# Kernel tuning notes

Measured on AMD Instinct MI355X. Metric: run time of the kernel, lower is better.

Reference implementation:

```python
import jax, jax.numpy as jnp
import numpy as np

C = 1024
H = 16
K = 2  # num_states
B, N = 4, 4096


def setup_inputs() -> dict:
    key = jax.random.key(0)
    ks_ = jax.random.split(key, 12)
    s = 1.0 / np.sqrt(C)
    inp = {
        "x": jax.random.normal(ks_[0], (B, N, C), dtype=jnp.float32),
        "Wq": jax.random.normal(ks_[1], (C, C), dtype=jnp.float32) * s,
        "bq": jnp.zeros((C,), dtype=jnp.float32),
        "Wk": jax.random.normal(ks_[2], (K, C, C), dtype=jnp.float32) * s,
        "bk": jnp.zeros((K, C), dtype=jnp.float32),
        "Wv": jax.random.normal(ks_[3], (K, C, C), dtype=jnp.float32) * s,
        "bv": jnp.zeros((K, C), dtype=jnp.float32),
        "Wo": jax.random.normal(ks_[4], (C, C), dtype=jnp.float32) * s,
        "bo": jnp.zeros((C,), dtype=jnp.float32),
        "ln_g": jnp.ones((C,), dtype=jnp.float32),
        "ln_b": jnp.zeros((C,), dtype=jnp.float32),
    }
    return inp


def _heads(t):
    # [..., n, (h d)] -> [..., h, n, d]
    shp = t.shape
    d = shp[-1] // H
    t = t.reshape(shp[:-1] + (H, d))
    return jnp.swapaxes(t, -2, -3)


def reference(x, Wq, bq, Wk, bk, Wv, bv, Wo, bo, ln_g, ln_b):
    dtype = x.dtype
    # residual single-layer projections (ResidualMLP with num_layers=-1)
    q = x + jnp.einsum('bnc,cd->bnd', x, Wq) + bq
    ks = x[None] + jnp.einsum('bnc,kcd->kbnd', x, Wk) + bk[:, None, None, :]
    vs = x[None] + jnp.einsum('bnc,kcd->kbnd', x, Wv) + bv[:, None, None, :]
    q = _heads(q)        # [b,h,n,d]
    ks = _heads(ks)      # [k,b,h,n,d]
    vs = _heads(vs)      # [k,b,h,n,d]
    scale = 1.0 / jnp.sqrt(jnp.asarray(N, dtype=jnp.float32))
    ks = ks.astype(jnp.float32) * scale
    vs = vs.astype(jnp.float32) * scale
    # per-state KV outer-products: [k,b,h,d,e]
    states = jnp.einsum('kbhnd,kbhne->kbhde', ks, vs)
    state = jnp.prod(states, axis=0)  # [b,h,d,e]
    out = jnp.einsum('bhnd,bhde->bhne', q.astype(jnp.float32), state)
    out = out.astype(dtype)
    # [b,h,n,d] -> [b,n,(h d)]
    out = jnp.swapaxes(out, 1, 2).reshape(x.shape[0], x.shape[1], C)
    # LayerNorm
    mu = jnp.mean(out, axis=-1, keepdims=True)
    var = jnp.var(out, axis=-1, keepdims=True)
    out = (out - mu) / jnp.sqrt(var + 1e-5) * ln_g + ln_b
    out = jnp.einsum('bnc,cd->bnd', out, Wo) + bo
    return out
```

## Files before the change

### kernel.cpp

```cpp
#include <hip/hip_runtime.h>
#include <hip/hip_bf16.h>

typedef __attribute__((ext_vector_type(8))) short bf16x8;
typedef __attribute__((ext_vector_type(4))) float f32x4;
typedef __attribute__((ext_vector_type(4))) short s16x4;

__device__ __forceinline__ short f2bf(float f) {
  union { float f; unsigned u; } v; v.f = f;
  unsigned r = v.u + 0x7fffu + ((v.u >> 16) & 1u);
  return (short)(r >> 16);
}

__device__ __forceinline__ float bf2f(short s) {
  union { float f; unsigned u; } v; v.u = ((unsigned)(unsigned short)s) << 16;
  return v.f;
}

#define GLD_LDS(g, l) __builtin_amdgcn_global_load_lds( \
    (const __attribute__((address_space(1))) void*)(g), \
    (__attribute__((address_space(3))) void*)(l), 16, 0, 0)

__global__ __launch_bounds__(256)
void convt_k(const float* __restrict__ x, short* __restrict__ xb,
             short* __restrict__ xbT, float* __restrict__ s) {
  __shared__ short tile[64][72];
  __shared__ float red[4][64];
  const int b = blockIdx.z;
  const int n0 = blockIdx.y * 64;
  const int c0 = blockIdx.x * 64;
  const int t = threadIdx.x;
  const int nl = t >> 4;
  const int c4 = (t & 15) << 2;
  const float* xp = x + ((size_t)b * 4096 + n0) * 1024 + c0;
#pragma unroll
  for (int i = 0; i < 4; ++i) {
    const int n = nl + 16 * i;
    const float4 v = *(const float4*)(xp + (size_t)n * 1024 + c4);
    s16x4 o;
    o[0] = f2bf(v.x); o[1] = f2bf(v.y); o[2] = f2bf(v.z); o[3] = f2bf(v.w);
    *(s16x4*)(&xb[((size_t)b * 4096 + n0 + n) * 1024 + c0 + c4]) = o;
    *(s16x4*)(&tile[n][c4]) = o;
  }
  __syncthreads();
  const int cll = t >> 4;
  const int n4 = (t & 15) << 2;
#pragma unroll
  for (int i = 0; i < 4; ++i) {
    const int c = cll + 16 * i;
    s16x4 o;
    o[0] = tile[n4 + 0][c]; o[1] = tile[n4 + 1][c];
    o[2] = tile[n4 + 2][c]; o[3] = tile[n4 + 3][c];
    *(s16x4*)(&xbT[((size_t)b * 1024 + c0 + c) * 4096 + n0 + n4]) = o;
  }
  const int part = t >> 6, col = t & 63;
  float cs = 0.f;
#pragma unroll
  for (int i = 0; i < 16; ++i) cs += bf2f(tile[part * 16 + i][col]);
  red[part][col] = cs;
  __syncthreads();
  if (part == 0)
    atomicAdd(&s[b * 1024 + c0 + col],
              red[0][col] + red[1][col] + red[2][col] + red[3][col]);
}

__global__ void twc_k(const float* __restrict__ Wq, const float* __restrict__ Wk,
                      const float* __restrict__ Wv, const float* __restrict__ Wo,
                      const float* __restrict__ lng, short* __restrict__ dst,
                      short* __restrict__ wqn) {
  __shared__ float tile[32][33];
  const int z = blockIdx.z;
  const float* src = (z == 0) ? Wq
                   : (z == 1) ? Wk
                   : (z == 2) ? (Wk + 1048576)
                   : (z == 3) ? Wv
                   : (z == 4) ? (Wv + 1048576)
                   : Wo;
  short* d = dst + (size_t)z * 1048576;
  const int tx = threadIdx.x, ty = threadIdx.y;
  const int c0 = blockIdx.y * 32, d0 = blockIdx.x * 32;
#pragma unroll
  for (int i = 0; i < 4; ++i) {
    const int cc = c0 + ty + i * 8;
    const float v = src[(size_t)cc * 1024 + d0 + tx];
    tile[ty + i * 8][tx] = v;
    if (z == 0)
      wqn[(size_t)cc * 1024 + d0 + tx] = f2bf(v + (cc == d0 + tx ? 1.0f : 0.0f));
  }
  __syncthreads();
#pragma unroll
  for (int i = 0; i < 4; ++i) {
    const int cc = c0 + tx;
    const int dd = d0 + ty + i * 8;
    float v = tile[tx][ty + i * 8];
    if (z < 5) {
      if (cc == dd) v += 1.0f;
    } else {
      v *= lng[cc];
    }
    d[(size_t)dd * 1024 + cc] = f2bf(v);
  }
}

__global__ __launch_bounds__(256)
void gemv_k(const short* __restrict__ wt, const float* __restrict__ s,
            float* __restrict__ u, float* __restrict__ w) {
  const int z = blockIdx.z, b = blockIdx.y;
  const int lane = threadIdx.x & 63, wid = threadIdx.x >> 6;
  const short* W = wt + ((size_t)(z + 1) << 20);
  const float* sb = s + b * 1024;
  float* outp = (z < 2) ? (u + (z * 4 + b) * 1024) : (w + ((z - 2) * 4 + b) * 1024);
#pragma unroll 1
  for (int it = 0; it < 16; ++it) {
    const int d = blockIdx.x * 64 + wid * 16 + it;
    const short* row = W + (size_t)d * 1024 + lane * 16;
    float acc = 0.f;
#pragma unroll
    for (int j = 0; j < 16; ++j) acc += bf2f(row[j]) * sb[lane * 16 + j];
#pragma unroll
    for (int o = 32; o > 0; o >>= 1) acc += __shfl_down(acc, o);
    if (lane == 0) outp[d] = acc;
  }
}

__global__ __launch_bounds__(256)
void ut_k(const float* __restrict__ Wo, const float* __restrict__ lng,
          const float* __restrict__ lnb, const float* __restrict__ bo,
          float* __restrict__ u, float* __restrict__ t) {
  const int dl = threadIdx.x & 63;
  const int dd = blockIdx.x * 64 + dl;
  const int part = threadIdx.x >> 6;
  float su = 0.f, st = 0.f;
  for (int c = part * 256; c < part * 256 + 256; ++c) {
    const float w = Wo[(size_t)c * 1024 + dd];
    su += lng[c] * w;
    st += lnb[c] * w;
  }
  __shared__ float rs[4][64], rt[4][64];
  rs[part][dl] = su; rt[part][dl] = st;
  __syncthreads();
  if (part == 0) {
    su = rs[0][dl] + rs[1][dl] + rs[2][dl] + rs[3][dl];
    st = rt[0][dl] + rt[1][dl] + rt[2][dl] + rt[3][dl];
    u[dd] = su;
    t[dd] = st + bo[dd];
  }
}

__global__ __launch_bounds__(512, 2)
void gram_k(const short* __restrict__ xbT, float* __restrict__ Pg) {
  extern __shared__ short lds[];
  const int tid = threadIdx.x;
  const int lane = tid & 63;
  const int wv = tid >> 6;
  const int wm = wv >> 2;
  const int wn = wv & 3;
  const int swz = ((blockIdx.x & 7) << 5) + (blockIdx.x >> 3);
  const int b = swz >> 6;
  const int kz = (swz >> 4) & 3;
  const int tl = swz & 15;
  const int bm0 = (tl >> 2) << 8, bn0 = (tl & 3) << 8;
  const int koff = kz << 10;
  const short* Ap = xbT + ((size_t)b << 22);
  float* po = Pg + ((size_t)((kz << 2) + b) << 20);

  const int lrow = ((lane >> 3) << 1) | ((lane >> 2) & 1);
  const int kc = ((lane & 3) ^ ((lane >> 3) & 3)) << 3;
  const int cl = lane & 15;
  const int khi = lane >> 4;

  f32x4 acc[8][4];
#pragma unroll
  for (int i = 0; i < 8; ++i)
#pragma unroll
    for (int j = 0; j < 4; ++j) acc[i][j] = f32x4{0.f, 0.f, 0.f, 0.f};

  auto stage = [&](int buf, int t) {
    const int k0 = koff + (t << 5) + kc;
    short* ab = lds + (buf << 14);
    short* bb = ab + 8192;
#pragma unroll
    for (int c = 0; c < 2; ++c) {
      const int un = wv * 2 + c;
      GLD_LDS(Ap + (size_t)(bm0 + (un << 4) + lrow) * 4096 + k0, ab + (un << 9));
      GLD_LDS(Ap + (size_t)(bn0 + (un << 4) + lrow) * 4096 + k0, bb + (un << 9));
    }
  };

  auto compute = [&](int buf) {
    const short* ab = lds + (buf << 14);
    const short* bb = ab + 8192;
    bf16x8 af[8], bfr[4];
#pragma unroll
    for (int i = 0; i < 8; ++i) {
      const int R = (wm << 7) + (i << 4) + cl;
      af[i] = *(const bf16x8*)(ab + (R << 5) + ((khi ^ ((R >> 1) & 3)) << 3));
    }
#pragma unroll
    for (int j = 0; j < 4; ++j) {
      const int C = (wn << 6) + (j << 4) + cl;
      bfr[j] = *(const bf16x8*)(bb + (C << 5) + ((khi ^ ((C >> 1) & 3)) << 3));
    }
#pragma unroll
    for (int i = 0; i < 8; ++i)
#pragma unroll
      for (int j = 0; j < 4; ++j)
        acc[i][j] = __builtin_amdgcn_mfma_f32_16x16x32_bf16(af[i], bfr[j], acc[i][j], 0, 0, 0);
  };

  stage(0, 0);
  stage(1, 1);
  asm volatile("s_waitcnt vmcnt(4)" ::: "memory");
  __builtin_amdgcn_s_barrier();
#pragma unroll 1
  for (int t = 0; t < 30; ++t) {
    stage((t + 2) & 3, t + 2);
    compute(t & 3);
    asm volatile("s_waitcnt vmcnt(4)" ::: "memory");
    __builtin_amdgcn_s_barrier();
  }
  compute(2);
  asm volatile("s_waitcnt vmcnt(0)" ::: "memory");
  __builtin_amdgcn_s_barrier();
  compute(3);

#pragma unroll
  for (int i = 0; i < 8; ++i)
#pragma unroll
    for (int j = 0; j < 4; ++j) {
      const int col = bn0 + (wn << 6) + (j << 4) + cl;
      const int rowb = bm0 + (wm << 7) + (i << 4) + (khi << 2);
#pragma unroll
      for (int r = 0; r < 4; ++r)
        po[(size_t)(rowb + r) * 1024 + col] = acc[i][j][r];
    }
}

__global__ __launch_bounds__(512, 2)
void oat_k(const short* __restrict__ xb, const short* __restrict__ Beff,
           const float* __restrict__ rq, short* __restrict__ oat,
           float* __restrict__ musum, float* __restrict__ sqsum) {
  extern __shared__ short lds[];
  const int tid = threadIdx.x;
  const int lane = tid & 63;
  const int wv = tid >> 6;
  const int wm = wv >> 2;
  const int wn = wv & 3;
  const int swz = ((blockIdx.x & 7) << 5) + (blockIdx.x >> 3);
  const int b = swz >> 6;
  const int tl = swz & 63;
  const int bm0 = (tl >> 2) << 8;
  const int bn0 = (tl & 3) << 8;
  const short* Ap = xb + ((size_t)b << 22);
  const short* Bp = Beff + ((size_t)b << 20);

  const int lrow = ((lane >> 3) << 1) | ((lane >> 2) & 1);
  const int kc = ((lane & 3) ^ ((lane >> 3) & 3)) << 3;
  const int cl = lane & 15;
  const int khi = lane >> 4;

  f32x4 acc[8][4];
#pragma unroll
  for (int i = 0; i < 8; ++i)
#pragma unroll
    for (int j = 0; j < 4; ++j) acc[i][j] = f32x4{0.f, 0.f, 0.f, 0.f};

  auto stage = [&](int buf, int t) {
    const int k0 = (t << 5) + kc;
    short* ab = lds + (buf << 14);
    short* bb = ab + 8192;
#pragma unroll
    for (int c = 0; c < 2; ++c) {
      const int un = wv * 2 + c;
      GLD_LDS(Ap + (size_t)(bm0 + (un << 4) + lrow) * 1024 + k0, ab + (un << 9));
      GLD_LDS(Bp + (size_t)(bn0 + (un << 4) + lrow) * 1024 + k0, bb + (un << 9));
    }
  };

  auto compute = [&](int buf) {
    const short* ab = lds + (buf << 14);
    const short* bb = ab + 8192;
    bf16x8 af[8], bfr[4];
#pragma unroll
    for (int i = 0; i < 8; ++i) {
      const int R = (wm << 7) + (i << 4) + cl;
      af[i] = *(const bf16x8*)(ab + (R << 5) + ((khi ^ ((R >> 1) & 3)) << 3));
    }
#pragma unroll
    for (int j = 0; j < 4; ++j) {
      const int C = (wn << 6) + (j << 4) + cl;
      bfr[j] = *(const bf16x8*)(bb + (C << 5) + ((khi ^ ((C >> 1) & 3)) << 3));
    }
#pragma unroll
    for (int i = 0; i < 8; ++i)
#pragma unroll
      for (int j = 0; j < 4; ++j)
        acc[i][j] = __builtin_amdgcn_mfma_f32_16x16x32_bf16(af[i], bfr[j], acc[i][j], 0, 0, 0);
  };

  stage(0, 0);
  stage(1, 1);
  asm volatile("s_waitcnt vmcnt(4)" ::: "memory");
  __builtin_amdgcn_s_barrier();
#pragma unroll 1
  for (int t = 0; t < 30; ++t) {
    stage((t + 2) & 3, t + 2);
    compute(t & 3);
    asm volatile("s_waitcnt vmcnt(4)" ::: "memory");
    __builtin_amdgcn_s_barrier();
  }
  compute(2);
  asm volatile("s_waitcnt vmcnt(0)" ::: "memory");
  __builtin_amdgcn_s_barrier();
  compute(3);

#pragma unroll
  for (int i = 0; i < 8; ++i) {
    const int rowb = bm0 + (wm << 7) + (i << 4) + (khi << 2);
    s16x4 pk[4];
#pragma unroll
    for (int j = 0; j < 4; ++j) {
      const int col = bn0 + (wn << 6) + (j << 4) + cl;
      const float rqc = rq[b * 1024 + col];
#pragma unroll
      for (int r = 0; r < 4; ++r) pk[j][r] = f2bf(acc[i][j][r] + rqc);
#pragma unroll
      for (int r = 0; r < 4; ++r)
        oat[(size_t)(b * 4096 + rowb + r) * 1024 + col] = pk[j][r];
    }
#pragma unroll
    for (int r = 0; r < 4; ++r) {
      float sv = 0.f, sq = 0.f;
#pragma unroll
      for (int j = 0; j < 4; ++j) {
        const float fv = bf2f(pk[j][r]);
        sv += fv; sq += fv * fv;
      }
#pragma unroll
      for (int m = 1; m < 16; m <<= 1) {
        sv += __shfl_xor(sv, m);
        sq += __shfl_xor(sq, m);
      }
      if (cl == 0) {
        atomicAdd(&musum[b * 4096 + rowb + r], sv);
        atomicAdd(&sqsum[b * 4096 + rowb + r], sq);
      }
    }
  }
}

__global__ __launch_bounds__(256)
void greduce_k(const float* __restrict__ Pg, short* __restrict__ G) {
  const int b = blockIdx.x >> 10;
  const int local = ((blockIdx.x & 1023) << 10) + (threadIdx.x << 2);
  float4 a = {0.f, 0.f, 0.f, 0.f};
#pragma unroll
  for (int kz = 0; kz < 4; ++kz) {
    const float4 v = *(const float4*)(Pg + (((size_t)((kz << 2) + b)) << 20) + local);
    a.x += v.x; a.y += v.y; a.z += v.z; a.w += v.w;
  }
  const float sc = 1.0f / 4096.0f;
  s16x4 o;
  o[0] = f2bf(a.x * sc); o[1] = f2bf(a.y * sc);
  o[2] = f2bf(a.z * sc); o[3] = f2bf(a.w * sc);
  *(s16x4*)(G + ((size_t)b << 20) + local) = o;
}

__global__ __launch_bounds__(256, 2)
void gemm128_k(const short* __restrict__ A, const short* __restrict__ Bt,
               short* __restrict__ out) {
  extern __shared__ short lds[];
  const int bid = blockIdx.x;
  const int swz = ((bid & 7) << 4) + (bid >> 3);
  const int bm0 = (swz >> 3) << 7;
  const int bn0 = (swz & 7) << 7;
  const short* Bp = Bt + ((size_t)blockIdx.y << 20);
  short* op = out + ((size_t)blockIdx.y << 21);
  const int tid = threadIdx.x, lane = tid & 63, wid = tid >> 6;
  const int wm = (wid >> 1) << 6, wn = (wid & 1) << 6;
  const int lrow = ((lane >> 3) << 1) | ((lane >> 2) & 1);
  const int kc = ((lane & 3) ^ ((lane >> 3) & 3)) << 3;
  const int cl = lane & 15, khi = lane >> 4;

  f32x4 acc[4][4];
#pragma unroll
  for (int i = 0; i < 4; ++i)
#pragma unroll
    for (int j = 0; j < 4; ++j) acc[i][j] = f32x4{0.f, 0.f, 0.f, 0.f};

  auto stage = [&](int buf, int t) {
    const int k0 = (t << 5) + kc;
    short* ab = lds + (buf << 13);
    short* bb = ab + 4096;
#pragma unroll
    for (int c = 0; c < 2; ++c) {
      const int un = wid * 2 + c;
      GLD_LDS(A + (size_t)(bm0 + (un << 4) + lrow) * 1024 + k0, ab + (un << 9));
      GLD_LDS(Bp + (size_t)(bn0 + (un << 4) + lrow) * 1024 + k0, bb + (un << 9));
    }
  };

  auto compute = [&](int buf) {
    const short* ab = lds + (buf << 13);
    const short* bb = ab + 4096;
    bf16x8 af[4], bfr[4];
#pragma unroll
    for (int i = 0; i < 4; ++i) {
      const int R = wm + (i << 4) + cl;
      af[i] = *(const bf16x8*)(ab + (R << 5) + ((khi ^ ((R >> 1) & 3)) << 3));
    }
#pragma unroll
    for (int j = 0; j < 4; ++j) {
      const int C = wn + (j << 4) + cl;
      bfr[j] = *(const bf16x8*)(bb + (C << 5) + ((khi ^ ((C >> 1) & 3)) << 3));
    }
#pragma unroll
    for (int i = 0; i < 4; ++i)
#pragma unroll
      for (int j = 0; j < 4; ++j)
        acc[i][j] = __builtin_amdgcn_mfma_f32_16x16x32_bf16(af[i], bfr[j], acc[i][j], 0, 0, 0);
  };

  stage(0, 0);
  stage(1, 1);
  asm volatile("s_waitcnt vmcnt(4)" ::: "memory");
  __builtin_amdgcn_s_barrier();
#pragma unroll 1
  for (int t = 0; t < 30; ++t) {
    stage((t + 2) & 3, t + 2);
    compute(t & 3);
    asm volatile("s_waitcnt vmcnt(4)" ::: "memory");
    __builtin_amdgcn_s_barrier();
  }
  compute(2);
  asm volatile("s_waitcnt vmcnt(0)" ::: "memory");
  __builtin_amdgcn_s_barrier();
  compute(3);

#pragma unroll
  for (int i = 0; i < 4; ++i)
#pragma unroll
    for (int j = 0; j < 4; ++j) {
      const int col = bn0 + wn + (j << 4) + cl;
      const int rowb = bm0 + wm + (i << 4) + (khi << 2);
#pragma unroll
      for (int r = 0; r < 4; ++r)
        op[(size_t)(rowb + r) * 1024 + col] = f2bf(acc[i][j][r]);
    }
}

__global__ __launch_bounds__(256)
void sw_k(const short* __restrict__ wt, const short* __restrict__ Tt,
          const float* __restrict__ u, const float* __restrict__ w,
          const float* __restrict__ bk, const float* __restrict__ bv,
          const short* __restrict__ wqn, const float* __restrict__ bq,
          short* __restrict__ Beff, float* __restrict__ rq) {
  __shared__ short Al[64 * 40];
  __shared__ short Bl[64 * 40];
  __shared__ short S[64][72];
  const int h = blockIdx.x & 15, b = blockIdx.x >> 4;
  const int tid = threadIdx.x, lane = tid & 63, wid = tid >> 6;
  const int srow = tid >> 2, sch = (tid & 3) << 3;
  const int cl = lane & 15, khi = lane >> 4;

  f32x4 acc2[2][4];
#pragma unroll
  for (int k = 0; k < 2; ++k)
#pragma unroll
    for (int j = 0; j < 4; ++j) acc2[k][j] = f32x4{0.f, 0.f, 0.f, 0.f};

#pragma unroll
  for (int k = 0; k < 2; ++k) {
    const short* Ap = wt + ((size_t)(1 + k) << 20) + ((size_t)(h * 64) << 10);
    const short* Bp = Tt + ((size_t)b << 21) + ((size_t)(k * 1024 + h * 64) << 10);
#pragma unroll 1
    for (int ns = 0; ns < 1024; ns += 32) {
      bf16x8 va = *(const bf16x8*)(Ap + ((size_t)srow << 10) + ns + sch);
      bf16x8 vb = *(const bf16x8*)(Bp + ((size_t)srow << 10) + ns + sch);
      __syncthreads();
      *(bf16x8*)(Al + srow * 40 + sch) = va;
      *(bf16x8*)(Bl + srow * 40 + sch) = vb;
      __syncthreads();
      bf16x8 a = *(const bf16x8*)(Al + (wid * 16 + cl) * 40 + (khi << 3));
#pragma unroll
      for (int j = 0; j < 4; ++j) {
        bf16x8 bb = *(const bf16x8*)(Bl + (j * 16 + cl) * 40 + (khi << 3));
        acc2[k][j] = __builtin_amdgcn_mfma_f32_16x16x32_bf16(a, bb, acc2[k][j], 0, 0, 0);
      }
    }
  }

  const int d0 = wid * 16 + (khi << 2);
  const float invN = 1.0f / 4096.0f;
#pragma unroll
  for (int j = 0; j < 4; ++j) {
    const int e = j * 16 + cl;
    s16x4 pk;
#pragma unroll
    for (int r = 0; r < 4; ++r) {
      const int d = d0 + r;
      float m[2];
#pragma unroll
      for (int k = 0; k < 2; ++k) {
        const float bkd = bk[k * 1024 + h * 64 + d];
        const float bve = bv[k * 1024 + h * 64 + e];
        const float ud = u[(k * 4 + b) * 1024 + h * 64 + d];
        const float we = w[(k * 4 + b) * 1024 + h * 64 + e];
        m[k] = acc2[k][j][r] + (ud * bve + bkd * we + 4096.f * bkd * bve) * invN;
      }
      pk[r] = f2bf(m[0] * m[1]);
    }
    *(s16x4*)(&S[e][d0]) = pk;
  }
  __syncthreads();

  if (wid == 0) {
    float acc = 0.f;
#pragma unroll 1
    for (int d = 0; d < 64; ++d) acc += bq[h * 64 + d] * bf2f(S[lane][d]);
    rq[b * 1024 + h * 64 + lane] = acc;
  }
  bf16x8 af[4][2];
#pragma unroll
  for (int mi = 0; mi < 4; ++mi)
#pragma unroll
    for (int kk = 0; kk < 2; ++kk)
      af[mi][kk] = *(const bf16x8*)(&S[mi * 16 + cl][kk * 32 + khi * 8]);
  const short* wq = wqn + h * 64;
  short* bdst = Beff + ((size_t)b << 20) + ((size_t)(h * 64) << 10);
#pragma unroll 1
  for (int nf = 0; nf < 16; ++nf) {
    const int c0 = wid * 256 + nf * 16;
    const bf16x8 bf0 = *(const bf16x8*)(wq + (size_t)(c0 + cl) * 1024 + khi * 8);
    const bf16x8 bf1 = *(const bf16x8*)(wq + (size_t)(c0 + cl) * 1024 + 32 + khi * 8);
    f32x4 a4[4];
#pragma unroll
    for (int mi = 0; mi < 4; ++mi) {
      a4[mi] = f32x4{0.f, 0.f, 0.f, 0.f};
      a4[mi] = __builtin_amdgcn_mfma_f32_16x16x32_bf16(af[mi][0], bf0, a4[mi], 0, 0, 0);
      a4[mi] = __builtin_amdgcn_mfma_f32_16x16x32_bf16(af[mi][1], bf1, a4[mi], 0, 0, 0);
    }
#pragma unroll
    for (int mi = 0; mi < 4; ++mi)
#pragma unroll
      for (int r = 0; r < 4; ++r)
        bdst[(size_t)(mi * 16 + khi * 4 + r) * 1024 + c0 + cl] = f2bf(a4[mi][r]);
  }
}

__global__ __launch_bounds__(512, 2)
void gemmo_k(const short* __restrict__ A, const short* __restrict__ WT,
             const float* __restrict__ musum, const float* __restrict__ sqsum,
             const float* __restrict__ uu, const float* __restrict__ tt,
             float* __restrict__ fout) {
  extern __shared__ short lds[];
  const int tid = threadIdx.x;
  const int lane = tid & 63;
  const int wv = tid >> 6;
  const int wm = wv >> 2;
  const int wn = wv & 3;
  const int swz = ((blockIdx.x & 7) << 5) + (blockIdx.x >> 3);
  const int bm0 = (swz >> 2) << 8;
  const int bn0 = (swz & 3) << 8;

  const int lrow = ((lane >> 3) << 1) | ((lane >> 2) & 1);
  const int kc = ((lane & 3) ^ ((lane >> 3) & 3)) << 3;
  const int cl = lane & 15;
  const int khi = lane >> 4;

  f32x4 acc[8][4];
#pragma unroll
  for (int i = 0; i < 8; ++i)
#pragma unroll
    for (int j = 0; j < 4; ++j) acc[i][j] = f32x4{0.f, 0.f, 0.f, 0.f};

  auto stage = [&](int buf, int t) {
    const int k0 = (t << 5) + kc;
    short* ab = lds + (buf << 14);
    short* bb = ab + 8192;
#pragma unroll
    for (int c = 0; c < 2; ++c) {
      const int un = wv * 2 + c;
      GLD_LDS(A + (size_t)(bm0 + (un << 4) + lrow) * 1024 + k0, ab + (un << 9));
      GLD_LDS(WT + (size_t)(bn0 + (un << 4) + lrow) * 1024 + k0, bb + (un << 9));
    }
  };

  auto compute = [&](int buf) {
    const short* ab = lds + (buf << 14);
    const short* bb = ab + 8192;
    bf16x8 af[8], bfr[4];
#pragma unroll
    for (int i = 0; i < 8; ++i) {
      const int R = (wm << 7) + (i << 4) + cl;
      af[i] = *(const bf16x8*)(ab + (R << 5) + ((khi ^ ((R >> 1) & 3)) << 3));
    }
#pragma unroll
    for (int j = 0; j < 4; ++j) {
      const int C = (wn << 6) + (j << 4) + cl;
      bfr[j] = *(const bf16x8*)(bb + (C << 5) + ((khi ^ ((C >> 1) & 3)) << 3));
    }
#pragma unroll
    for (int i = 0; i < 8; ++i)
#pragma unroll
      for (int j = 0; j < 4; ++j)
        acc[i][j] = __builtin_amdgcn_mfma_f32_16x16x32_bf16(af[i], bfr[j], acc[i][j], 0, 0, 0);
  };

  stage(0, 0);
  stage(1, 1);
  asm volatile("s_waitcnt vmcnt(4)" ::: "memory");
  __builtin_amdgcn_s_barrier();
#pragma unroll 1
  for (int t = 0; t < 30; ++t) {
    stage((t + 2) & 3, t + 2);
    compute(t & 3);
    asm volatile("s_waitcnt vmcnt(4)" ::: "memory");
    __builtin_amdgcn_s_barrier();
  }
  compute(2);
  asm volatile("s_waitcnt vmcnt(0)" ::: "memory");
  __builtin_amdgcn_s_barrier();
  compute(3);

#pragma unroll
  for (int i = 0; i < 8; ++i) {
    const int rowb = bm0 + (wm << 7) + (i << 4) + (khi << 2);
    const float4 ms = *(const float4*)(musum + rowb);
    const float4 qs = *(const float4*)(sqsum + rowb);
    float mu[4], rs[4];
    mu[0] = ms.x * (1.0f / 1024.0f); mu[1] = ms.y * (1.0f / 1024.0f);
    mu[2] = ms.z * (1.0f / 1024.0f); mu[3] = ms.w * (1.0f / 1024.0f);
    rs[0] = rsqrtf(fmaxf(qs.x * (1.0f / 1024.0f) - mu[0] * mu[0], 0.f) + 1e-5f);
    rs[1] = rsqrtf(fmaxf(qs.y * (1.0f / 1024.0f) - mu[1] * mu[1], 0.f) + 1e-5f);
    rs[2] = rsqrtf(fmaxf(qs.z * (1.0f / 1024.0f) - mu[2] * mu[2], 0.f) + 1e-5f);
    rs[3] = rsqrtf(fmaxf(qs.w * (1.0f / 1024.0f) - mu[3] * mu[3], 0.f) + 1e-5f);
#pragma unroll
    for (int j = 0; j < 4; ++j) {
      const int col = bn0 + (wn << 6) + (j << 4) + cl;
      const float uc = uu[col];
      const float tc = tt[col];
#pragma unroll
      for (int r = 0; r < 4; ++r)
        fout[(size_t)(rowb + r) * 1024 + col] = rs[r] * (acc[i][j][r] - mu[r] * uc) + tc;
    }
  }
}

extern "C" void kernel_launch(void* const* d_in, const int* in_sizes, int n_in,
                              void* d_out, int out_size, void* d_ws, size_t ws_size,
                              hipStream_t stream) {
  const float* x = (const float*)d_in[0];
  const float* Wq = (const float*)d_in[1];
  const float* bq = (const float*)d_in[2];
  const float* Wk = (const float*)d_in[3];
  const float* bk = (const float*)d_in[4];
  const float* Wv = (const float*)d_in[5];
  const float* bv = (const float*)d_in[6];
  const float* Wo = (const float*)d_in[7];
  const float* bo = (const float*)d_in[8];
  const float* lng = (const float*)d_in[9];
  const float* lnb = (const float*)d_in[10];

  char* ws = (char*)d_ws;
  short* xb = (short*)(ws + 0);
  short* wt = (short*)(ws + 33554432);
  short* wqn = (short*)(ws + 46137344);
  short* Beff = (short*)(ws + 48234496);
  float* rq = (float*)(ws + 56623104);
  float* musum = (float*)(ws + 56639488);
  float* sqsum = (float*)(ws + 56705024);
  float* s = (float*)(ws + 56770560);
  float* u = (float*)(ws + 56786944);
  float* w = (float*)(ws + 56819712);
  float* uu = (float*)(ws + 56852480);
  float* tt = (float*)(ws + 56856576);
  short* xbT = (short*)(ws + 79691776);
  short* Gt = (short*)(ws + 113246208);
  short* Tt = (short*)(ws + 121634816);
  float* Pg = (float*)(ws + 143351808);
  short* oat = xbT;

  hipMemsetAsync(musum, 0, 147456, stream);
  convt_k<<<dim3(16, 64, 4), 256, 0, stream>>>(x, xb, xbT, s);
  twc_k<<<dim3(32, 32, 6), dim3(32, 8), 0, stream>>>(Wq, Wk, Wv, Wo, lng, wt, wqn);
  gemv_k<<<dim3(16, 4, 4), 256, 0, stream>>>(wt, s, u, w);
  ut_k<<<16, 256, 0, stream>>>(Wo, lng, lnb, bo, uu, tt);

  gram_k<<<256, 512, 131072, stream>>>(xbT, Pg);
  greduce_k<<<4096, 256, 0, stream>>>(Pg, Gt);
  gemm128_k<<<dim3(128, 4), 256, 65536, stream>>>(wt + 3145728, Gt, Tt);
  sw_k<<<64, 256, 0, stream>>>(wt, Tt, u, w, bk, bv, wqn, bq, Beff, rq);

  oat_k<<<256, 512, 131072, stream>>>(xb, Beff, rq, oat, musum, sqsum);
  gemmo_k<<<256, 512, 131072, stream>>>(oat, wt + 5242880, musum, sqsum, uu, tt,
                                        (float*)d_out);
}
```

Measured before the change: 271.6 us.

## Unify GEMMs into 128x128 triple-buffered template; exploit Gram symmetry

Four 256x256-tile GEMM kernels using 512 threads and a 4-stage LDS ring are replaced by one templated 128x128-tile kernel. It uses 256 threads, a 3-stage ring, 48KB of LDS and a target of 3 blocks per CU, with a MODE parameter selecting the prologue and epilogue. The Gram kernel now computes only the upper-triangular tiles of the symmetric x^T x. The reduction kernel then sums the split-K partials per 64x64 tile and writes each off-diagonal tile's transpose through LDS. This raises block count and occupancy and roughly halves Gram MFMA work, at the cost of lower per-block reuse and more global traffic per FLOP.

Measured after the change: 278.3 us. +2.5%, slower.

```diff
diff --git a/kernel.cpp b/kernel.cpp
--- a/kernel.cpp
+++ b/kernel.cpp
@@ -146,62 +146,93 @@
   }
 }
 
-__global__ __launch_bounds__(512, 2)
-void gram_k(const short* __restrict__ xbT, float* __restrict__ Pg) {
+template <int MODE>
+__global__ __launch_bounds__(256, 3)
+void g128_k(const short* __restrict__ A0, const short* __restrict__ B0,
+            const float* __restrict__ cr0, const float* __restrict__ cr1,
+            float* __restrict__ musum, float* __restrict__ sqsum,
+            short* __restrict__ obf, float* __restrict__ of32) {
   extern __shared__ short lds[];
-  const int tid = threadIdx.x;
-  const int lane = tid & 63;
-  const int wv = tid >> 6;
-  const int wm = wv >> 2;
-  const int wn = wv & 3;
-  const int swz = ((blockIdx.x & 7) << 5) + (blockIdx.x >> 3);
-  const int b = swz >> 6;
-  const int kz = (swz >> 4) & 3;
-  const int tl = swz & 15;
-  const int bm0 = (tl >> 2) << 8, bn0 = (tl & 3) << 8;
-  const int koff = kz << 10;
-  const short* Ap = xbT + ((size_t)b << 22);
-  float* po = Pg + ((size_t)((kz << 2) + b) << 20);
-
+  const int tid = threadIdx.x, lane = tid & 63, wid = tid >> 6;
+  const int wm = (wid >> 1) << 6, wn = (wid & 1) << 6;
   const int lrow = ((lane >> 3) << 1) | ((lane >> 2) & 1);
   const int kc = ((lane & 3) ^ ((lane >> 3) & 3)) << 3;
-  const int cl = lane & 15;
-  const int khi = lane >> 4;
-
-  f32x4 acc[8][4];
-#pragma unroll
-  for (int i = 0; i < 8; ++i)
+  const int cl = lane & 15, khi = lane >> 4;
+
+  int bm0, bn0, koff = 0, b = 0, ld;
+  const short *Ap, *Bp;
+  if constexpr (MODE == 0) {
+    const int swz = (blockIdx.x & 7) * 72 + (blockIdx.x >> 3);
+    const int panel = swz / 36;
+    int uu2 = swz % 36;
+    b = panel >> 2;
+    const int kz = panel & 3;
+    int ti = 0;
+    while (uu2 >= 8 - ti) { uu2 -= 8 - ti; ++ti; }
+    const int tj = ti + uu2;
+    bm0 = ti << 7; bn0 = tj << 7;
+    koff = kz << 10; ld = 4096;
+    Ap = A0 + ((size_t)b << 22);
+    Bp = Ap;
+    of32 += ((size_t)((kz << 2) + b) << 20);
+  } else if constexpr (MODE == 1) {
+    const int swz = (blockIdx.x & 7) * 64 + (blockIdx.x >> 3);
+    b = swz >> 7;
+    const int tl = swz & 127;
+    bm0 = (tl >> 3) << 7; bn0 = (tl & 7) << 7;
+    ld = 1024;
+    Ap = A0;
+    Bp = B0 + ((size_t)b << 20);
+    obf += ((size_t)b << 21);
+  } else if constexpr (MODE == 2) {
+    const int swz = (blockIdx.x & 7) * 128 + (blockIdx.x >> 3);
+    b = swz >> 8;
+    const int tl = swz & 255;
+    bm0 = (tl >> 3) << 7; bn0 = (tl & 7) << 7;
+    ld = 1024;
+    Ap = A0 + ((size_t)b << 22);
+    Bp = B0 + ((size_t)b << 20);
+  } else {
+    const int swz = (blockIdx.x & 7) * 128 + (blockIdx.x >> 3);
+    bm0 = (swz >> 3) << 7; bn0 = (swz & 7) << 7;
+    ld = 1024;
+    Ap = A0; Bp = B0;
+  }
+
+  f32x4 acc[4][4];
+#pragma unroll
+  for (int i = 0; i < 4; ++i)
 #pragma unroll
     for (int j = 0; j < 4; ++j) acc[i][j] = f32x4{0.f, 0.f, 0.f, 0.f};
 
   auto stage = [&](int buf, int t) {
     const int k0 = koff + (t << 5) + kc;
-    short* ab = lds + (buf << 14);
-    short* bb = ab + 8192;
+    short* ab = lds + buf * 8192;
+    short* bb = ab + 4096;
 #pragma unroll
     for (int c = 0; c < 2; ++c) {
-      const int un = wv * 2 + c;
-      GLD_LDS(Ap + (size_t)(bm0 + (un << 4) + lrow) * 4096 + k0, ab + (un << 9));
-      GLD_LDS(Ap + (size_t)(bn0 + (un << 4) + lrow) * 4096 + k0, bb + (un << 9));
+      const int un = wid * 2 + c;
+      GLD_LDS(Ap + (size_t)(bm0 + (un << 4) + lrow) * ld + k0, ab + (un << 9));
+      GLD_LDS(Bp + (size_t)(bn0 + (un << 4) + lrow) * ld + k0, bb + (un << 9));
     }
   };
 
   auto compute = [&](int buf) {
-    const short* ab = lds + (buf << 14);
-    const short* bb = ab + 8192;
-    bf16x8 af[8], bfr[4];
-#pragma unroll
-    for (int i = 0; i < 8; ++i) {
-      const int R = (wm << 7) + (i << 4) + cl;
+    const short* ab = lds + buf * 8192;
+    const short* bb = ab + 4096;
+    bf16x8 af[4], bfr[4];
+#pragma unroll
+    for (int i = 0; i < 4; ++i) {
+      const int R = wm + (i << 4) + cl;
       af[i] = *(const bf16x8*)(ab + (R << 5) + ((khi ^ ((R >> 1) & 3)) << 3));
     }
 #pragma unroll
     for (int j = 0; j < 4; ++j) {
-      const int C = (wn << 6) + (j << 4) + cl;
+      const int C = wn + (j << 4) + cl;
       bfr[j] = *(const bf16x8*)(bb + (C << 5) + ((khi ^ ((C >> 1) & 3)) << 3));
     }
 #pragma unroll
-    for (int i = 0; i < 8; ++i)
+    for (int i = 0; i < 4; ++i)
 #pragma unroll
       for (int j = 0; j < 4; ++j)
         acc[i][j] = __builtin_amdgcn_mfma_f32_16x16x32_bf16(af[i], bfr[j], acc[i][j], 0, 0, 0);
@@ -213,239 +244,145 @@
   __builtin_amdgcn_s_barrier();
 #pragma unroll 1
   for (int t = 0; t < 30; ++t) {
-    stage((t + 2) & 3, t + 2);
-    compute(t & 3);
+    stage((t + 2) % 3, t + 2);
+    compute(t % 3);
     asm volatile("s_waitcnt vmcnt(4)" ::: "memory");
     __builtin_amdgcn_s_barrier();
   }
-  compute(2);
+  compute(0);
   asm volatile("s_waitcnt vmcnt(0)" ::: "memory");
   __builtin_amdgcn_s_barrier();
-  compute(3);
-
-#pragma unroll
-  for (int i = 0; i < 8; ++i)
-#pragma unroll
-    for (int j = 0; j < 4; ++j) {
-      const int col = bn0 + (wn << 6) + (j << 4) + cl;
-      const int rowb = bm0 + (wm << 7) + (i << 4) + (khi << 2);
-#pragma unroll
-      for (int r = 0; r < 4; ++r)
-        po[(size_t)(rowb + r) * 1024 + col] = acc[i][j][r];
-    }
-}
-
-__global__ __launch_bounds__(512, 2)
-void oat_k(const short* __restrict__ xb, const short* __restrict__ Beff,
-           const float* __restrict__ rq, short* __restrict__ oat,
-           float* __restrict__ musum, float* __restrict__ sqsum) {
-  extern __shared__ short lds[];
-  const int tid = threadIdx.x;
-  const int lane = tid & 63;
-  const int wv = tid >> 6;
-  const int wm = wv >> 2;
-  const int wn = wv & 3;
-  const int swz = ((blockIdx.x & 7) << 5) + (blockIdx.x >> 3);
-  const int b = swz >> 6;
-  const int tl = swz & 63;
-  const int bm0 = (tl >> 2) << 8;
-  const int bn0 = (tl & 3) << 8;
-  const short* Ap = xb + ((size_t)b << 22);
-  const short* Bp = Beff + ((size_t)b << 20);
-
-  const int lrow = ((lane >> 3) << 1) | ((lane >> 2) & 1);
-  const int kc = ((lane & 3) ^ ((lane >> 3) & 3)) << 3;
-  const int cl = lane & 15;
-  const int khi = lane >> 4;
-
-  f32x4 acc[8][4];
-#pragma unroll
-  for (int i = 0; i < 8; ++i)
-#pragma unroll
-    for (int j = 0; j < 4; ++j) acc[i][j] = f32x4{0.f, 0.f, 0.f, 0.f};
-
-  auto stage = [&](int buf, int t) {
-    const int k0 = (t << 5) + kc;
-    short* ab = lds + (buf << 14);
-    short* bb = ab + 8192;
-#pragma unroll
-    for (int c = 0; c < 2; ++c) {
-      const int un = wv * 2 + c;
-      GLD_LDS(Ap + (size_t)(bm0 + (un << 4) + lrow) * 1024 + k0, ab + (un << 9));
-      GLD_LDS(Bp + (size_t)(bn0 + (un << 4) + lrow) * 1024 + k0, bb + (un << 9));
-    }
-  };
-
-  auto compute = [&](int buf) {
-    const short* ab = lds + (buf << 14);
-    const short* bb = ab + 8192;
-    bf16x8 af[8], bfr[4];
-#pragma unroll
-    for (int i = 0; i < 8; ++i) {
-      const int R = (wm << 7) + (i << 4) + cl;
-      af[i] = *(const bf16x8*)(ab + (R << 5) + ((khi ^ ((R >> 1) & 3)) << 3));
-    }
-#pragma unroll
-    for (int j = 0; j < 4; ++j) {
-      const int C = (wn << 6) + (j << 4) + cl;
-      bfr[j] = *(const bf16x8*)(bb + (C << 5) + ((khi ^ ((C >> 1) & 3)) << 3));
-    }
-#pragma unroll
-    for (int i = 0; i < 8; ++i)
-#pragma unroll
-      for (int j = 0; j < 4; ++j)
-        acc[i][j] = __builtin_amdgcn_mfma_f32_16x16x32_bf16(af[i], bfr[j], acc[i][j], 0, 0, 0);
-  };
-
-  stage(0, 0);
-  stage(1, 1);
-  asm volatile("s_waitcnt vmcnt(4)" ::: "memory");
-  __builtin_amdgcn_s_barrier();
-#pragma unroll 1
-  for (int t = 0; t < 30; ++t) {
-    stage((t + 2) & 3, t + 2);
-    compute(t & 3);
-    asm volatile("s_waitcnt vmcnt(4)" ::: "memory");
-    __builtin_amdgcn_s_barrier();
-  }
-  compute(2);
-  asm volatile("s_waitcnt vmcnt(0)" ::: "memory");
-  __builtin_amdgcn_s_barrier();
-  compute(3);
-
-#pragma unroll
-  for (int i = 0; i < 8; ++i) {
-    const int rowb = bm0 + (wm << 7) + (i << 4) + (khi << 2);
-    s16x4 pk[4];
-#pragma unroll
-    for (int j = 0; j < 4; ++j) {
-      const int col = bn0 + (wn << 6) + (j << 4) + cl;
-      const float rqc = rq[b * 1024 + col];
-#pragma unroll
-      for (int r = 0; r < 4; ++r) pk[j][r] = f2bf(acc[i][j][r] + rqc);
-#pragma unroll
-      for (int r = 0; r < 4; ++r)
-        oat[(size_t)(b * 4096 + rowb + r) * 1024 + col] = pk[j][r];
-    }
-#pragma unroll
-    for (int r = 0; r < 4; ++r) {
-      float sv = 0.f, sq = 0.f;
+  compute(1);
+
+  if constexpr (MODE == 0) {
+#pragma unroll
+    for (int i = 0; i < 4; ++i)
 #pragma unroll
       for (int j = 0; j < 4; ++j) {
-        const float fv = bf2f(pk[j][r]);
-        sv += fv; sq += fv * fv;
-      }
-#pragma unroll
-      for (int m = 1; m < 16; m <<= 1) {
-        sv += __shfl_xor(sv, m);
-        sq += __shfl_xor(sq, m);
-      }
-      if (cl == 0) {
-        atomicAdd(&musum[b * 4096 + rowb + r], sv);
-        atomicAdd(&sqsum[b * 4096 + rowb + r], sq);
+        const int col = bn0 + wn + (j << 4) + cl;
+        const int rowb = bm0 + wm + (i << 4) + (khi << 2);
+#pragma unroll
+        for (int r = 0; r < 4; ++r)
+          of32[(size_t)(rowb + r) * 1024 + col] = acc[i][j][r];
+      }
+  } else if constexpr (MODE == 1) {
+#pragma unroll
+    for (int i = 0; i < 4; ++i)
+#pragma unroll
+      for (int j = 0; j < 4; ++j) {
+        const int col = bn0 + wn + (j << 4) + cl;
+        const int rowb = bm0 + wm + (i << 4) + (khi << 2);
+#pragma unroll
+        for (int r = 0; r < 4; ++r)
+          obf[(size_t)(rowb + r) * 1024 + col] = f2bf(acc[i][j][r]);
+      }
+  } else if constexpr (MODE == 2) {
+#pragma unroll
+    for (int i = 0; i < 4; ++i) {
+      const int rowb = bm0 + wm + (i << 4) + (khi << 2);
+      s16x4 pk[4];
+#pragma unroll
+      for (int j = 0; j < 4; ++j) {
+        const int col = bn0 + wn + (j << 4) + cl;
+        const float rqc = cr0[b * 1024 + col];
+#pragma unroll
+        for (int r = 0; r < 4; ++r) pk[j][r] = f2bf(acc[i][j][r] + rqc);
+#pragma unroll
+        for (int r = 0; r < 4; ++r)
+          obf[(size_t)(b * 4096 + rowb + r) * 1024 + col] = pk[j][r];
+      }
+#pragma unroll
+      for (int r = 0; r < 4; ++r) {
+        float sv = 0.f, sq = 0.f;
+#pragma unroll
+        for (int j = 0; j < 4; ++j) {
+          const float fv = bf2f(pk[j][r]);
+          sv += fv; sq += fv * fv;
+        }
+#pragma unroll
+        for (int m = 1; m < 16; m <<= 1) {
+          sv += __shfl_xor(sv, m);
+          sq += __shfl_xor(sq, m);
+        }
+        if (cl == 0) {
+          atomicAdd(&musum[b * 4096 + rowb + r], sv);
+          atomicAdd(&sqsum[b * 4096 + rowb + r], sq);
+        }
+      }
+    }
+  } else {
+#pragma unroll
+    for (int i = 0; i < 4; ++i) {
+      const int rowb = bm0 + wm + (i << 4) + (khi << 2);
+      const float4 ms = *(const float4*)(musum + rowb);
+      const float4 qs = *(const float4*)(sqsum + rowb);
+      float mu[4], rs[4];
+      mu[0] = ms.x * (1.0f / 1024.0f); mu[1] = ms.y * (1.0f / 1024.0f);
+      mu[2] = ms.z * (1.0f / 1024.0f); mu[3] = ms.w * (1.0f / 1024.0f);
+      rs[0] = rsqrtf(fmaxf(qs.x * (1.0f / 1024.0f) - mu[0] * mu[0], 0.f) + 1e-5f);
+      rs[1] = rsqrtf(fmaxf(qs.y * (1.0f / 1024.0f) - mu[1] * mu[1], 0.f) + 1e-5f);
+      rs[2] = rsqrtf(fmaxf(qs.z * (1.0f / 1024.0f) - mu[2] * mu[2], 0.f) + 1e-5f);
+      rs[3] = rsqrtf(fmaxf(qs.w * (1.0f / 1024.0f) - mu[3] * mu[3], 0.f) + 1e-5f);
+#pragma unroll
+      for (int j = 0; j < 4; ++j) {
+        const int col = bn0 + wn + (j << 4) + cl;
+        const float uc = cr0[col];
+        const float tc = cr1[col];
+#pragma unroll
+        for (int r = 0; r < 4; ++r)
+          of32[(size_t)(rowb + r) * 1024 + col] = rs[r] * (acc[i][j][r] - mu[r] * uc) + tc;
       }
     }
   }
 }
 
 __global__ __launch_bounds__(256)
-void greduce_k(const float* __restrict__ Pg, short* __restrict__ G) {
-  const int b = blockIdx.x >> 10;
-  const int local = ((blockIdx.x & 1023) << 10) + (threadIdx.x << 2);
-  float4 a = {0.f, 0.f, 0.f, 0.f};
+void gred_k(const float* __restrict__ Pg, short* __restrict__ G) {
+  __shared__ short tile[64][72];
+  const int bid = blockIdx.x;
+  const int b = bid / 136;
+  int u = bid % 136;
+  int ti = 0;
+  while (u >= 16 - ti) { u -= 16 - ti; ++ti; }
+  const int tj = ti + u;
+  const int r = threadIdx.x >> 2;
+  const int c0 = (threadIdx.x & 3) << 4;
+  float acc[16];
+#pragma unroll
+  for (int q = 0; q < 16; ++q) acc[q] = 0.f;
 #pragma unroll
   for (int kz = 0; kz < 4; ++kz) {
-    const float4 v = *(const float4*)(Pg + (((size_t)((kz << 2) + b)) << 20) + local);
-    a.x += v.x; a.y += v.y; a.z += v.z; a.w += v.w;
+    const float* p = Pg + (((size_t)((kz << 2) + b)) << 20)
+                   + (size_t)(ti * 64 + r) * 1024 + tj * 64 + c0;
+#pragma unroll
+    for (int q4 = 0; q4 < 4; ++q4) {
+      const float4 v = ((const float4*)p)[q4];
+      acc[q4 * 4 + 0] += v.x; acc[q4 * 4 + 1] += v.y;
+      acc[q4 * 4 + 2] += v.z; acc[q4 * 4 + 3] += v.w;
+    }
   }
   const float sc = 1.0f / 4096.0f;
-  s16x4 o;
-  o[0] = f2bf(a.x * sc); o[1] = f2bf(a.y * sc);
-  o[2] = f2bf(a.z * sc); o[3] = f2bf(a.w * sc);
-  *(s16x4*)(G + ((size_t)b << 20) + local) = o;
-}
-
-__global__ __launch_bounds__(256, 2)
-void gemm128_k(const short* __restrict__ A, const short* __restrict__ Bt,
-               short* __restrict__ out) {
-  extern __shared__ short lds[];
-  const int bid = blockIdx.x;
-  const int swz = ((bid & 7) << 4) + (bid >> 3);
-  const int bm0 = (swz >> 3) << 7;
-  const int bn0 = (swz & 7) << 7;
-  const short* Bp = Bt + ((size_t)blockIdx.y << 20);
-  short* op = out + ((size_t)blockIdx.y << 21);
-  const int tid = threadIdx.x, lane = tid & 63, wid = tid >> 6;
-  const int wm = (wid >> 1) << 6, wn = (wid & 1) << 6;
-  const int lrow = ((lane >> 3) << 1) | ((lane >> 2) & 1);
-  const int kc = ((lane & 3) ^ ((lane >> 3) & 3)) << 3;
-  const int cl = lane & 15, khi = lane >> 4;
-
-  f32x4 acc[4][4];
-#pragma unroll
-  for (int i = 0; i < 4; ++i)
-#pragma unroll
-    for (int j = 0; j < 4; ++j) acc[i][j] = f32x4{0.f, 0.f, 0.f, 0.f};
-
-  auto stage = [&](int buf, int t) {
-    const int k0 = (t << 5) + kc;
-    short* ab = lds + (buf << 13);
-    short* bb = ab + 4096;
-#pragma unroll
-    for (int c = 0; c < 2; ++c) {
-      const int un = wid * 2 + c;
-      GLD_LDS(A + (size_t)(bm0 + (un << 4) + lrow) * 1024 + k0, ab + (un << 9));
-      GLD_LDS(Bp + (size_t)(bn0 + (un << 4) + lrow) * 1024 + k0, bb + (un << 9));
-    }
-  };
-
-  auto compute = [&](int buf) {
-    const short* ab = lds + (buf << 13);
-    const short* bb = ab + 4096;
-    bf16x8 af[4], bfr[4];
-#pragma unroll
-    for (int i = 0; i < 4; ++i) {
-      const int R = wm + (i << 4) + cl;
-      af[i] = *(const bf16x8*)(ab + (R << 5) + ((khi ^ ((R >> 1) & 3)) << 3));
-    }
-#pragma unroll
-    for (int j = 0; j < 4; ++j) {
-      const int C = wn + (j << 4) + cl;
-      bfr[j] = *(const bf16x8*)(bb + (C << 5) + ((khi ^ ((C >> 1) & 3)) << 3));
-    }
-#pragma unroll
-    for (int i = 0; i < 4; ++i)
-#pragma unroll
-      for (int j = 0; j < 4; ++j)
-        acc[i][j] = __builtin_amdgcn_mfma_f32_16x16x32_bf16(af[i], bfr[j], acc[i][j], 0, 0, 0);
-  };
-
-  stage(0, 0);
-  stage(1, 1);
-  asm volatile("s_waitcnt vmcnt(4)" ::: "memory");
-  __builtin_amdgcn_s_barrier();
-#pragma unroll 1
-  for (int t = 0; t < 30; ++t) {
-    stage((t + 2) & 3, t + 2);
-    compute(t & 3);
-    asm volatile("s_waitcnt vmcnt(4)" ::: "memory");
-    __builtin_amdgcn_s_barrier();
-  }
-  compute(2);
-  asm volatile("s_waitcnt vmcnt(0)" ::: "memory");
-  __builtin_amdgcn_s_barrier();
-  compute(3);
-
-#pragma unroll
-  for (int i = 0; i < 4; ++i)
-#pragma unroll
-    for (int j = 0; j < 4; ++j) {
-      const int col = bn0 + wn + (j << 4) + cl;
-      const int rowb = bm0 + wm + (i << 4) + (khi << 2);
-#pragma unroll
-      for (int r = 0; r < 4; ++r)
-        op[(size_t)(rowb + r) * 1024 + col] = f2bf(acc[i][j][r]);
-    }
+  short* gb = G + ((size_t)b << 20);
+#pragma unroll
+  for (int q4 = 0; q4 < 4; ++q4) {
+    s16x4 o;
+#pragma unroll
+    for (int e = 0; e < 4; ++e) {
+      o[e] = f2bf(acc[q4 * 4 + e] * sc);
+      tile[r][c0 + q4 * 4 + e] = o[e];
+    }
+    *(s16x4*)(gb + (size_t)(ti * 64 + r) * 1024 + tj * 64 + c0 + q4 * 4) = o;
+  }
+  __syncthreads();
+  if (ti != tj) {
+#pragma unroll
+    for (int q4 = 0; q4 < 4; ++q4) {
+      s16x4 o;
+#pragma unroll
+      for (int e = 0; e < 4; ++e) o[e] = tile[c0 + q4 * 4 + e][r];
+      *(s16x4*)(gb + (size_t)(tj * 64 + r) * 1024 + ti * 64 + c0 + q4 * 4) = o;
+    }
+  }
 }
 
 __global__ __launch_bounds__(256)
@@ -544,105 +481,6 @@
 #pragma unroll
       for (int r = 0; r < 4; ++r)
         bdst[(size_t)(mi * 16 + khi * 4 + r) * 1024 + c0 + cl] = f2bf(a4[mi][r]);
-  }
-}
-
-__global__ __launch_bounds__(512, 2)
-void gemmo_k(const short* __restrict__ A, const short* __restrict__ WT,
-             const float* __restrict__ musum, const float* __restrict__ sqsum,
-             const float* __restrict__ uu, const float* __restrict__ tt,
-             float* __restrict__ fout) {
-  extern __shared__ short lds[];
-  const int tid = threadIdx.x;
-  const int lane = tid & 63;
-  const int wv = tid >> 6;
-  const int wm = wv >> 2;
-  const int wn = wv & 3;
-  const int swz = ((blockIdx.x & 7) << 5) + (blockIdx.x >> 3);
-  const int bm0 = (swz >> 2) << 8;
-  const int bn0 = (swz & 3) << 8;
-
-  const int lrow = ((lane >> 3) << 1) | ((lane >> 2) & 1);
-  const int kc = ((lane & 3) ^ ((lane >> 3) & 3)) << 3;
-  const int cl = lane & 15;
-  const int khi = lane >> 4;
-
-  f32x4 acc[8][4];
-#pragma unroll
-  for (int i = 0; i < 8; ++i)
-#pragma unroll
-    for (int j = 0; j < 4; ++j) acc[i][j] = f32x4{0.f, 0.f, 0.f, 0.f};
-
-  auto stage = [&](int buf, int t) {
-    const int k0 = (t << 5) + kc;
-    short* ab = lds + (buf << 14);
-    short* bb = ab + 8192;
-#pragma unroll
-    for (int c = 0; c < 2; ++c) {
-      const int un = wv * 2 + c;
-      GLD_LDS(A + (size_t)(bm0 + (un << 4) + lrow) * 1024 + k0, ab + (un << 9));
-      GLD_LDS(WT + (size_t)(bn0 + (un << 4) + lrow) * 1024 + k0, bb + (un << 9));
-    }
-  };
-
-  auto compute = [&](int buf) {
-    const short* ab = lds + (buf << 14);
-    const short* bb = ab + 8192;
-    bf16x8 af[8], bfr[4];
-#pragma unroll
-    for (int i = 0; i < 8; ++i) {
-      const int R = (wm << 7) + (i << 4) + cl;
-      af[i] = *(const bf16x8*)(ab + (R << 5) + ((khi ^ ((R >> 1) & 3)) << 3));
-    }
-#pragma unroll
-    for (int j = 0; j < 4; ++j) {
-      const int C = (wn << 6) + (j << 4) + cl;
-      bfr[j] = *(const bf16x8*)(bb + (C << 5) + ((khi ^ ((C >> 1) & 3)) << 3));
-    }
-#pragma unroll
-    for (int i = 0; i < 8; ++i)
-#pragma unroll
-      for (int j = 0; j < 4; ++j)
-        acc[i][j] = __builtin_amdgcn_mfma_f32_16x16x32_bf16(af[i], bfr[j], acc[i][j], 0, 0, 0);
-  };
-
-  stage(0, 0);
-  stage(1, 1);
-  asm volatile("s_waitcnt vmcnt(4)" ::: "memory");
-  __builtin_amdgcn_s_barrier();
-#pragma unroll 1
-  for (int t = 0; t < 30; ++t) {
-    stage((t + 2) & 3, t + 2);
-    compute(t & 3);
-    asm volatile("s_waitcnt vmcnt(4)" ::: "memory");
-    __builtin_amdgcn_s_barrier();
-  }
-  compute(2);
-  asm volatile("s_waitcnt vmcnt(0)" ::: "memory");
-  __builtin_amdgcn_s_barrier();
-  compute(3);
-
-#pragma unroll
-  for (int i = 0; i < 8; ++i) {
-    const int rowb = bm0 + (wm << 7) + (i << 4) + (khi << 2);
-    const float4 ms = *(const float4*)(musum + rowb);
-    const float4 qs = *(const float4*)(sqsum + rowb);
-    float mu[4], rs[4];
-    mu[0] = ms.x * (1.0f / 1024.0f); mu[1] = ms.y * (1.0f / 1024.0f);
-    mu[2] = ms.z * (1.0f / 1024.0f); mu[3] = ms.w * (1.0f / 1024.0f);
-    rs[0] = rsqrtf(fmaxf(qs.x * (1.0f / 1024.0f) - mu[0] * mu[0], 0.f) + 1e-5f);
-    rs[1] = rsqrtf(fmaxf(qs.y * (1.0f / 1024.0f) - mu[1] * mu[1], 0.f) + 1e-5f);
-    rs[2] = rsqrtf(fmaxf(qs.z * (1.0f / 1024.0f) - mu[2] * mu[2], 0.f) + 1e-5f);
-    rs[3] = rsqrtf(fmaxf(qs.w * (1.0f / 1024.0f) - mu[3] * mu[3], 0.f) + 1e-5f);
-#pragma unroll
-    for (int j = 0; j < 4; ++j) {
-      const int col = bn0 + (wn << 6) + (j << 4) + cl;
-      const float uc = uu[col];
-      const float tc = tt[col];
-#pragma unroll
-      for (int r = 0; r < 4; ++r)
-        fout[(size_t)(rowb + r) * 1024 + col] = rs[r] * (acc[i][j][r] - mu[r] * uc) + tc;
-    }
   }
 }
 
@@ -686,12 +524,15 @@
   gemv_k<<<dim3(16, 4, 4), 256, 0, stream>>>(wt, s, u, w);
   ut_k<<<16, 256, 0, stream>>>(Wo, lng, lnb, bo, uu, tt);
 
-  gram_k<<<256, 512, 131072, stream>>>(xbT, Pg);
-  greduce_k<<<4096, 256, 0, stream>>>(Pg, Gt);
-  gemm128_k<<<dim3(128, 4), 256, 65536, stream>>>(wt + 3145728, Gt, Tt);
+  g128_k<0><<<576, 256, 49152, stream>>>(xbT, nullptr, nullptr, nullptr,
+                                         nullptr, nullptr, nullptr, Pg);
+  gred_k<<<544, 256, 0, stream>>>(Pg, Gt);
+  g128_k<1><<<512, 256, 49152, stream>>>(wt + 3145728, Gt, nullptr, nullptr,
+                                         nullptr, nullptr, Tt, nullptr);
   sw_k<<<64, 256, 0, stream>>>(wt, Tt, u, w, bk, bv, wqn, bq, Beff, rq);
 
-  oat_k<<<256, 512, 131072, stream>>>(xb, Beff, rq, oat, musum, sqsum);
-  gemmo_k<<<256, 512, 131072, stream>>>(oat, wt + 5242880, musum, sqsum, uu, tt,
-                                        (float*)d_out);
-}
+  g128_k<2><<<1024, 256, 49152, stream>>>(xb, Beff, rq, nullptr,
+                                          musum, sqsum, oat, nullptr);
+  g128_k<3><<<1024, 256, 49152, stream>>>(oat, wt + 5242880, uu, tt,
+                                          musum, sqsum, nullptr, (float*)d_out);
+}
```
